# Kernel tuning notes

Measured on AMD Instinct MI355X. Metric: run time of the kernel, lower is better.

Reference implementation:

```python
import jax, jax.numpy as jnp
import numpy as np

T, A = 4096, 4          # tokens, atoms per token
N = T * A               # flat atoms
QB, KB = 32, 128        # query block / key window (AF3 atom transformer)
S = N // QB             # number of query subsets
H, DK = 4, 32           # heads, key dim per head
NB = 3                  # transformer blocks
CA, CP, CT = 128, 16, 384

# clipped sliding key window centered on each 32-atom query block
KIDX = jnp.clip(jnp.arange(S)[:, None] * QB - (KB - QB) // 2 + jnp.arange(KB)[None, :], 0, N - 1)

PARAM_SHAPES = [('w_ref_pos', (3, CA)), ('w_ref_mask', (1, CA)), ('w_ref_element', (CA, CA)), ('w_ref_charge', (1, CA)), ('w_ref_atom_name', (256, CA)), ('w_s2p_row', (CA, CP)), ('w_s2p_col', (CA, CP)), ('w_pair_offsets', (3, CP)), ('w_pair_dist', (1, CP)), ('w_pair_mask', (1, CP)), ('w_pair_mlp1', (CP, CP)), ('w_pair_mlp2', (CP, CP)), ('w_pair_mlp3', (CP, CP)), ('w_pair_ln', (CP,)), ('w_pair_logits', (CP, NB * H)), ('aq_lnw', (NB, CA)), ('aq_gw', (NB, CA, CA)), ('aq_gb', (NB, CA)), ('aq_sw', (NB, CA, CA)), ('ak_lnw', (NB, CA)), ('ak_gw', (NB, CA, CA)), ('ak_gb', (NB, CA)), ('ak_sw', (NB, CA, CA)), ('wq', (NB, CA, CA)), ('bq', (NB, CA)), ('wk', (NB, CA, CA)), ('wv', (NB, CA, CA)), ('wg', (NB, CA, CA)), ('azi_w', (NB, CA, CA)), ('azi_cw', (NB, CA, CA)), ('azi_cb', (NB, CA)), ('t_lnw', (NB, CA)), ('t_gw', (NB, CA, CA)), ('t_gb', (NB, CA)), ('t_sw', (NB, CA, CA)), ('glu1', (NB, CA, 2 * CA)), ('glu2', (NB, CA, 2 * CA)), ('t_azi_w', (NB, 2 * CA, CA)), ('t_azi_cw', (NB, CA, CA)), ('t_azi_cb', (NB, CA)), ('w_project', (CA, CT))]


def _ln(x, w=None, eps=1e-5):
    mu = jnp.mean(x, -1, keepdims=True)
    var = jnp.var(x, -1, keepdims=True)
    xn = (x - mu) * jax.lax.rsqrt(var + eps)
    return xn * w if w is not None else xn


def _ada_ln(x, cond, lnw, gw, gb, sw):
    c = _ln(cond, lnw)
    return jax.nn.sigmoid(c @ gw + gb) * _ln(x) + c @ sw


def setup_inputs() -> dict:
    ks = iter(jax.random.split(jax.random.key(0), 64))
    d = {}
    d['positions'] = jax.random.normal(next(ks), (T, A, 3), jnp.float32) * 3.0
    d['mask'] = jnp.ones((T, A), jnp.float32)
    d['element'] = jax.random.randint(next(ks), (T, A), 0, 128, jnp.int32)
    d['charge'] = jax.random.normal(next(ks), (T, A), jnp.float32)
    d['atom_name_chars'] = jax.random.randint(next(ks), (T, A, 4), 0, 64, jnp.int32)
    d['ref_space_uid'] = jax.random.randint(next(ks), (T, A), 0, T, jnp.int32)
    for nm, shp in PARAM_SHAPES:
        if nm.endswith('lnw') or nm == 'w_pair_ln':
            d[nm] = jnp.ones(shp, jnp.float32)
        else:
            d[nm] = jax.random.normal(next(ks), shp, jnp.float32) * 0.02
    return d


def _forward(positions, mask, charge, w_ref_pos, w_ref_mask, w_ref_element, w_ref_charge, w_ref_atom_name, w_s2p_row, w_s2p_col, w_pair_offsets, w_pair_dist, w_pair_mask, w_pair_mlp1, w_pair_mlp2, w_pair_mlp3, w_pair_ln, w_pair_logits, aq_lnw, aq_gw, aq_gb, aq_sw, ak_lnw, ak_gw, ak_gb, ak_sw, wq, bq, wk, wv, wg, azi_w, azi_cw, azi_cb, t_lnw, t_gw, t_gb, t_sw, glu1, glu2, t_azi_w, t_azi_cw, t_azi_cb, w_project, element, atom_name_chars, ref_space_uid):
    dt = positions.dtype
    pos = positions.reshape(N, 3)
    m = mask.reshape(N, 1)
    # per_atom_cond
    el1h = jax.nn.one_hot(element.reshape(N), 128, dtype=dt)
    nm1h = jax.nn.one_hot(atom_name_chars.reshape(N, 4), 64, dtype=dt).reshape(N, 256)
    ch = jnp.arcsinh(charge.reshape(N, 1))
    act = pos @ w_ref_pos + m @ w_ref_mask + el1h @ w_ref_element + ch @ w_ref_charge + nm1h @ w_ref_atom_name
    act = act * m
    qsc = act.reshape(S, QB, CA)  # queries_single_cond
    # pair conditioning
    uid = ref_space_uid.reshape(N)
    q_uid, k_uid = uid.reshape(S, QB), uid[KIDX]
    q_pos, k_pos = pos.reshape(S, QB, 3), pos[KIDX]
    valid = (q_uid[:, :, None] == k_uid[:, None, :]).astype(dt)[..., None]  # [S,QB,KB,1]
    off = q_pos[:, :, None, :] - k_pos[:, None, :, :]  # [S,QB,KB,3]
    pair = (off @ w_pair_offsets) * valid
    sq = jnp.sum(off * off, -1, keepdims=True)
    pair = pair + ((1.0 / (1.0 + sq)) @ w_pair_dist) * valid
    ksc = act[KIDX]  # keys_single_cond [S,KB,CA]
    pair = pair + (jax.nn.relu(qsc) @ w_s2p_row)[:, :, None, :] + (jax.nn.relu(ksc) @ w_s2p_col)[:, None, :, :]
    pair = pair + valid @ w_pair_mask
    t = jax.nn.relu(pair) @ w_pair_mlp1
    t = jax.nn.relu(t) @ w_pair_mlp2
    t = jax.nn.relu(t) @ w_pair_mlp3
    pair = pair + t
    # pair logits for all blocks: [NB, S, H, QB, KB]
    pl = (_ln(pair, w_pair_ln) @ w_pair_logits).reshape(S, QB, KB, NB, H)
    pl = jnp.transpose(pl, (3, 0, 4, 1, 2))
    qact = qsc
    scale = DK ** -0.5
    for i in range(NB):
        kact = qact.reshape(N, CA)[KIDX]
        xq = _ada_ln(qact, qsc, aq_lnw[i], aq_gw[i], aq_gb[i], aq_sw[i])
        xk = _ada_ln(kact, ksc, ak_lnw[i], ak_gw[i], ak_gb[i], ak_sw[i])
        q = (xq @ wq[i] + bq[i]).reshape(S, QB, H, DK)
        k = (xk @ wk[i]).reshape(S, KB, H, DK)
        logits = jnp.einsum('sqhd,skhd->shqk', q * scale, k) + pl[i]
        aw = jax.nn.softmax(logits, axis=-1)
        v = (xk @ wv[i]).reshape(S, KB, H, DK)
        o = jnp.einsum('shqk,skhd->sqhd', aw, v).reshape(S, QB, CA)
        o = o * jax.nn.sigmoid(xq @ wg[i])
        o = (o @ azi_w[i]) * jax.nn.sigmoid(qsc @ azi_cw[i] + azi_cb[i])  # AdaptiveZeroInit
        qact = qact + o
        xt = _ada_ln(qact, qsc, t_lnw[i], t_gw[i], t_gb[i], t_sw[i])
        xt = jax.nn.silu(xt @ glu1[i]) * (xt @ glu2[i])  # SwiGLU
        xt = (xt @ t_azi_w[i]) * jax.nn.sigmoid(qsc @ t_azi_cw[i] + t_azi_cb[i])
        qact = qact + xt
    tok = jax.nn.relu(qact.reshape(T, A, CA) @ w_project)
    mm = mask[..., None]
    token_act = jnp.sum(tok * mm, -2) / jnp.maximum(jnp.sum(mm, -2), 1e-10)
    return token_act, qact, qsc, pair


def reference(positions, mask, element, charge, atom_name_chars, ref_space_uid, w_ref_pos, w_ref_mask, w_ref_element, w_ref_charge, w_ref_atom_name, w_s2p_row, w_s2p_col, w_pair_offsets, w_pair_dist, w_pair_mask, w_pair_mlp1, w_pair_mlp2, w_pair_mlp3, w_pair_ln, w_pair_logits, aq_lnw, aq_gw, aq_gb, aq_sw, ak_lnw, ak_gw, ak_gb, ak_sw, wq, bq, wk, wv, wg, azi_w, azi_cw, azi_cb, t_lnw, t_gw, t_gb, t_sw, glu1, glu2, t_azi_w, t_azi_cw, t_azi_cb, w_project):
    return _forward(positions, mask, charge, w_ref_pos, w_ref_mask, w_ref_element, w_ref_charge, w_ref_atom_name, w_s2p_row, w_s2p_col, w_pair_offsets, w_pair_dist, w_pair_mask, w_pair_mlp1, w_pair_mlp2, w_pair_mlp3, w_pair_ln, w_pair_logits, aq_lnw, aq_gw, aq_gb, aq_sw, ak_lnw, ak_gw, ak_gb, ak_sw, wq, bq, wk, wv, wg, azi_w, azi_cw, azi_cb, t_lnw, t_gw, t_gb, t_sw, glu1, glu2, t_azi_w, t_azi_cw, t_azi_cb, w_project, element, atom_name_chars, ref_space_uid)
```

## Files before the change

kernel.cpp:

```cpp
#include <hip/hip_runtime.h>
#include <math.h>

#define TT 4096
#define AA 4
#define NN 16384
#define QBQ 32
#define KBK 128
#define SS 512
#define HH 4
#define DKD 32
#define CAC 128
#define CPC 16
#define CTC 384

typedef __attribute__((ext_vector_type(8))) short bf16x8;
typedef __attribute__((ext_vector_type(4))) short s16x4;
typedef __attribute__((ext_vector_type(4))) float f32x4;

__device__ __forceinline__ float sig_(float x) { return 1.0f / (1.0f + __expf(-x)); }
__device__ __forceinline__ short f2bf(float f) {
    unsigned u = __float_as_uint(f);
    unsigned r = (u + 0x7FFFu + ((u >> 16) & 1u)) >> 16;
    return (short)r;
}
__device__ __forceinline__ float b2f(short s) {
    return __uint_as_float(((unsigned)(unsigned short)s) << 16);
}

struct PEnt { const float* src; const float* rs; short* dst; int K; int NC; };
struct PTab { PEnt e[49]; };

__global__ __launch_bounds__(256) void k_prep(PTab tab)
{
    const PEnt e = tab.e[blockIdx.y];
    const int ntx = e.NC >> 5, nty = e.K >> 5, nt = ntx * nty;
    __shared__ float sm[32][33];
    const int lx = threadIdx.x & 31, ly = threadIdx.x >> 5;
    for (int t = blockIdx.x; t < nt; t += gridDim.x) {
        const int ty = t / ntx, tx = t - ty * ntx;
        #pragma unroll
        for (int j = 0; j < 4; ++j) {
            const int k = ty * 32 + ly + j * 8;
            const int n = tx * 32 + lx;
            float v = e.src[(size_t)k * e.NC + n];
            if (e.rs) v *= e.rs[k];
            sm[ly + j * 8][lx] = v;
        }
        __syncthreads();
        #pragma unroll
        for (int j = 0; j < 4; ++j) {
            const int n = tx * 32 + ly + j * 8;
            const int k = ty * 32 + lx;
            e.dst[(size_t)n * e.K + k] = f2bf(sm[lx][ly + j * 8]);
        }
        __syncthreads();
    }
}

__global__ __launch_bounds__(128) void k_atom_cond(
    const float* __restrict__ pos, const float* __restrict__ msk,
    const int* __restrict__ elem, const float* __restrict__ chg,
    const int* __restrict__ chars,
    const float* __restrict__ w_pos, const float* __restrict__ w_msk,
    const float* __restrict__ w_elem, const float* __restrict__ w_chg,
    const float* __restrict__ w_name,
    const float* __restrict__ w_row, const float* __restrict__ w_col,
    float* __restrict__ qsc, float* __restrict__ qact,
    short* __restrict__ qsc_bf, short* __restrict__ qn_bf,
    float* __restrict__ stats,
    float* __restrict__ rq, float* __restrict__ rk)
{
    const int n = blockIdx.x, c = threadIdx.x;
    const float p0 = pos[n*3+0], p1 = pos[n*3+1], p2 = pos[n*3+2];
    const float m = msk[n];
    const int   el = elem[n];
    const float ach = asinhf(chg[n]);
    const int c0 = chars[n*4+0], c1 = chars[n*4+1], c2 = chars[n*4+2], c3 = chars[n*4+3];

    float a = p0*w_pos[c] + p1*w_pos[CAC+c] + p2*w_pos[2*CAC+c]
            + m*w_msk[c] + w_elem[el*CAC+c] + ach*w_chg[c]
            + w_name[(c0      )*CAC+c] + w_name[( 64+c1)*CAC+c]
            + w_name[(128+c2)*CAC+c] + w_name[(192+c3)*CAC+c];
    a *= m;

    const size_t base = (size_t)n*CAC + c;
    qsc[base] = a; qact[base] = a; qsc_bf[base] = f2bf(a);

    __shared__ float red[128];
    __shared__ float sh[128];
    red[c] = a; __syncthreads();
    for (int off = 64; off > 0; off >>= 1) { if (c < off) red[c] += red[c+off]; __syncthreads(); }
    const float mu = red[0] * (1.0f/128.0f);
    __syncthreads();
    const float d = a - mu;
    red[c] = d*d; __syncthreads();
    for (int off = 64; off > 0; off >>= 1) { if (c < off) red[c] += red[c+off]; __syncthreads(); }
    const float var = red[0] * (1.0f/128.0f);
    const float rs = rsqrtf(var + 1e-5f);
    qn_bf[base] = f2bf(d * rs);
    if (c == 0) { stats[2*n] = mu; stats[2*n+1] = rs; }
    __syncthreads();
    sh[c] = fmaxf(a, 0.0f);
    __syncthreads();
    if (c < 32) {
        const float* w = (c < 16) ? w_row : w_col;
        const int cc = c & 15;
        float acc = 0.0f;
        #pragma unroll 8
        for (int r = 0; r < 128; ++r) acc += sh[r] * w[r*CPC + cc];
        if (c < 16) rq[(size_t)n*CPC + cc] = acc;
        else        rk[(size_t)n*CPC + cc] = acc;
    }
}

__global__ __launch_bounds__(256) void k_pair(
    const float* __restrict__ pos, const int* __restrict__ uid,
    const float* __restrict__ rq, const float* __restrict__ rk,
    const float* __restrict__ w_ofs, const float* __restrict__ w_dist,
    const float* __restrict__ w_pm,
    const float* __restrict__ mlp1, const float* __restrict__ mlp2,
    const float* __restrict__ mlp3,
    const float* __restrict__ wln, const float* __restrict__ wpl,
    float* __restrict__ pair, short* __restrict__ plb)
{
    __shared__ float sm1[256], sm2[256], sm3[256], sofs[48], sdist[16], smask[16];
    __shared__ float swln[16], swpl[192];
    const int tid = threadIdx.x;
    sm1[tid] = mlp1[tid]; sm2[tid] = mlp2[tid]; sm3[tid] = mlp3[tid];
    if (tid < 48) sofs[tid] = w_ofs[tid];
    if (tid < 16) { sdist[tid] = w_dist[tid]; smask[tid] = w_pm[tid]; swln[tid] = wln[tid]; }
    if (tid < 192) swpl[tid] = wpl[tid];
    __syncthreads();

    const int gid = blockIdx.x*256 + tid;
    const int s = gid >> 12;
    const int rem = gid & 4095;
    const int q = rem >> 7, kk = rem & 127;
    const int n = s*QBQ + q;
    int kidx = s*QBQ - 48 + kk; kidx = max(0, min(NN-1, kidx));

    const float v = (uid[n] == uid[kidx]) ? 1.0f : 0.0f;
    const float o0 = pos[n*3+0]-pos[kidx*3+0];
    const float o1 = pos[n*3+1]-pos[kidx*3+1];
    const float o2 = pos[n*3+2]-pos[kidx*3+2];
    const float sq = o0*o0 + o1*o1 + o2*o2;
    const float inv = 1.0f/(1.0f + sq);

    const float* rqp = rq + (size_t)n*CPC;
    const float* rkp = rk + (size_t)kidx*CPC;

    float p[16], t1[16], t2[16];
    #pragma unroll
    for (int j = 0; j < 16; ++j)
        p[j] = v*(o0*sofs[j] + o1*sofs[16+j] + o2*sofs[32+j] + inv*sdist[j] + smask[j])
             + rqp[j] + rkp[j];
    #pragma unroll
    for (int j = 0; j < 16; ++j) {
        float acc = 0.0f;
        #pragma unroll
        for (int r = 0; r < 16; ++r) acc += fmaxf(p[r], 0.0f) * sm1[r*16+j];
        t1[j] = acc;
    }
    #pragma unroll
    for (int j = 0; j < 16; ++j) {
        float acc = 0.0f;
        #pragma unroll
        for (int r = 0; r < 16; ++r) acc += fmaxf(t1[r], 0.0f) * sm2[r*16+j];
        t2[j] = acc;
    }
    #pragma unroll
    for (int j = 0; j < 16; ++j) {
        float acc = 0.0f;
        #pragma unroll
        for (int r = 0; r < 16; ++r) acc += fmaxf(t2[r], 0.0f) * sm3[r*16+j];
        t1[j] = p[j] + acc;
    }
    float* op = pair + (size_t)gid*CPC;
    #pragma unroll
    for (int j = 0; j < 4; ++j)
        *(float4*)(op + j*4) = make_float4(t1[j*4], t1[j*4+1], t1[j*4+2], t1[j*4+3]);

    float sm = 0.0f;
    #pragma unroll
    for (int j = 0; j < 16; ++j) sm += t1[j];
    const float mu = sm * (1.0f/16.0f);
    float vq = 0.0f;
    #pragma unroll
    for (int j = 0; j < 16; ++j) { const float dd = t1[j]-mu; vq += dd*dd; }
    const float rs = rsqrtf(vq*(1.0f/16.0f) + 1e-5f);
    float xn[16];
    #pragma unroll
    for (int j = 0; j < 16; ++j) xn[j] = (t1[j]-mu)*rs*swln[j];
    #pragma unroll
    for (int i = 0; i < 3; ++i) {
        #pragma unroll
        for (int h = 0; h < 4; ++h) {
            float acc = 0.0f;
            #pragma unroll
            for (int j = 0; j < 16; ++j) acc += xn[j] * swpl[j*12 + i*4 + h];
            plb[((((size_t)i*SS + s)*HH + h)*QBQ + q)*KBK + kk] = f2bf(acc);
        }
    }
}

struct FJob {
    const void* A; const void* A2;
    const float* stats; const short* G; const short* S;
    const short* Bt; const float* bias;
    float* outF; short* outB;
    const short* gate; float* resid; float* ostats;
    int K; int ostride; int amode; int emode;
};
struct FJobs { FJob j[8]; };

__global__ __launch_bounds__(256) void k_mmf(FJobs jobs)
{
    __shared__ short As[128*64];
    __shared__ short Bs[128*64];
    const FJob J = jobs.j[blockIdx.y];
    const int tid = threadIdx.x;
    const int wave = tid >> 6, lane = tid & 63;
    const int l15 = lane & 15, l4 = lane >> 4;
    const int row0 = blockIdx.x * 128;
    const int K = J.K;

    f32x4 acc[2][8];
    #pragma unroll
    for (int m = 0; m < 2; ++m)
        #pragma unroll
        for (int n = 0; n < 8; ++n) acc[m][n] = (f32x4){0.f,0.f,0.f,0.f};

    for (int k0 = 0; k0 < K; k0 += 64) {
        #pragma unroll
        for (int j = 0; j < 4; ++j) {
            const int u = tid + j*256;
            const int r = u >> 3, ug = u & 7;
            const int row = row0 + r;
            const size_t ao = (size_t)row*K + k0 + ug*8;
            bf16x8 av;
            if (J.amode == 0) {
                av = *(const bf16x8*)((const short*)J.A + ao);
            } else if (J.amode == 1) {
                const float* Af = (const float*)J.A;
                const float4 a0 = *(const float4*)(Af + ao);
                const float4 a1 = *(const float4*)(Af + ao + 4);
                const float mu = J.stats[2*row], rs = J.stats[2*row+1];
                const s16x4 g0 = *(const s16x4*)(J.G + ao), g1 = *(const s16x4*)(J.G + ao + 4);
                const s16x4 s0 = *(const s16x4*)(J.S + ao), s1 = *(const s16x4*)(J.S + ao + 4);
                const float x[8] = {a0.x,a0.y,a0.z,a0.w,a1.x,a1.y,a1.z,a1.w};
                #pragma unroll
                for (int t = 0; t < 4; ++t) {
                    av[t]   = f2bf(b2f(g0[t])*((x[t]  -mu)*rs) + b2f(s0[t]));
                    av[t+4] = f2bf(b2f(g1[t])*((x[t+4]-mu)*rs) + b2f(s1[t]));
                }
            } else if (J.amode == 2) {
                const float* Ao = (const float*)J.A;
                const float* Ag = (const float*)J.A2;
                const float4 oa = *(const float4*)(Ao + ao);
                const float4 ob = *(const float4*)(Ao + ao + 4);
                const float4 ga = *(const float4*)(Ag + ao);
                const float4 gb = *(const float4*)(Ag + ao + 4);
                av[0]=f2bf(oa.x*ga.x); av[1]=f2bf(oa.y*ga.y); av[2]=f2bf(oa.z*ga.z); av[3]=f2bf(oa.w*ga.w);
                av[4]=f2bf(ob.x*gb.x); av[5]=f2bf(ob.y*gb.y); av[6]=f2bf(ob.z*gb.z); av[7]=f2bf(ob.w*gb.w);
            } else {
                const float* Af = (const float*)J.A;
                const float4 a0 = *(const float4*)(Af + ao);
                const float4 a1 = *(const float4*)(Af + ao + 4);
                av[0]=f2bf(a0.x); av[1]=f2bf(a0.y); av[2]=f2bf(a0.z); av[3]=f2bf(a0.w);
                av[4]=f2bf(a1.x); av[5]=f2bf(a1.y); av[6]=f2bf(a1.z); av[7]=f2bf(a1.w);
            }
            *(bf16x8*)&As[r*64 + ((ug ^ (r & 7)) * 8)] = av;
            const bf16x8 bv = *(const bf16x8*)(J.Bt + (size_t)r*K + k0 + ug*8);
            *(bf16x8*)&Bs[r*64 + ((ug ^ (r & 7)) * 8)] = bv;
        }
        __syncthreads();
        #pragma unroll
        for (int ks = 0; ks < 2; ++ks) {
            bf16x8 af[2], bfr[8];
            #pragma unroll
            for (int m = 0; m < 2; ++m) {
                const int r = wave*32 + m*16 + l15;
                af[m] = *(const bf16x8*)&As[r*64 + (((ks*4 + l4) ^ (r & 7)) * 8)];
            }
            #pragma unroll
            for (int n = 0; n < 8; ++n) {
                const int c = n*16 + l15;
                bfr[n] = *(const bf16x8*)&Bs[c*64 + (((ks*4 + l4) ^ (c & 7)) * 8)];
            }
            #pragma unroll
            for (int m = 0; m < 2; ++m)
                #pragma unroll
                for (int n = 0; n < 8; ++n)
                    acc[m][n] = __builtin_amdgcn_mfma_f32_16x16x32_bf16(af[m], bfr[n], acc[m][n], 0, 0, 0);
        }
        __syncthreads();
    }

    if (J.emode == 3) {
        #pragma unroll
        for (int m = 0; m < 2; ++m) {
            #pragma unroll
            for (int reg = 0; reg < 4; ++reg) {
                const int row = row0 + wave*32 + m*16 + l4*4 + reg;
                float s = 0.0f, q = 0.0f;
                #pragma unroll
                for (int n = 0; n < 8; ++n) {
                    const int col = n*16 + l15;
                    const size_t off = (size_t)row*CAC + col;
                    const float v = J.resid[off] + acc[m][n][reg] * b2f(J.gate[off]);
                    J.resid[off] = v;
                    s += v; q += v*v;
                }
                #pragma unroll
                for (int msk = 1; msk < 16; msk <<= 1) {
                    s += __shfl_xor(s, msk, 64);
                    q += __shfl_xor(q, msk, 64);
                }
                if (l15 == 0) {
                    const float mu = s * (1.0f/128.0f);
                    const float var = q * (1.0f/128.0f) - mu*mu;
                    J.ostats[2*row]   = mu;
                    J.ostats[2*row+1] = rsqrtf(var + 1e-5f);
                }
            }
        }
    } else {
        float bval[8];
        #pragma unroll
        for (int n = 0; n < 8; ++n) bval[n] = 0.0f;
        if (J.bias) {
            #pragma unroll
            for (int n = 0; n < 8; ++n) bval[n] = J.bias[n*16 + l15];
        }
        const int epi = J.emode;
        #pragma unroll
        for (int m = 0; m < 2; ++m) {
            #pragma unroll
            for (int n = 0; n < 8; ++n) {
                const int col = n*16 + l15;
                #pragma unroll
                for (int reg = 0; reg < 4; ++reg) {
                    const int row = row0 + wave*32 + m*16 + l4*4 + reg;
                    float v = acc[m][n][reg] + bval[n];
                    if (epi == 1) v = sig_(v);
                    if (epi == 2) v = fmaxf(v, 0.0f);
                    if (J.outB) J.outB[(size_t)row*J.ostride + col] = f2bf(v);
                    else        J.outF[(size_t)row*J.ostride + col] = v;
                }
            }
        }
    }
}

__global__ __launch_bounds__(256) void k_mm_glu(
    const float* __restrict__ qact, const float* __restrict__ stats,
    const short* __restrict__ Gt, const short* __restrict__ St,
    const short* __restrict__ B1t, const short* __restrict__ B2t,
    short* __restrict__ out)
{
    __shared__ short As[128*64];
    __shared__ short B1s[64*64];
    __shared__ short B2s[64*64];
    const int tid = threadIdx.x;
    const int wave = tid >> 6, lane = tid & 63;
    const int l15 = lane & 15, l4 = lane >> 4;
    const int row0 = blockIdx.x * 128;
    const int col0 = blockIdx.y * 64;

    f32x4 acc1[2][4], acc2[2][4];
    #pragma unroll
    for (int m = 0; m < 2; ++m)
        #pragma unroll
        for (int n = 0; n < 4; ++n) {
            acc1[m][n] = (f32x4){0.f,0.f,0.f,0.f};
            acc2[m][n] = (f32x4){0.f,0.f,0.f,0.f};
        }

    for (int k0 = 0; k0 < 128; k0 += 64) {
        #pragma unroll
        for (int j = 0; j < 4; ++j) {
            const int u = tid + j*256;
            const int r = u >> 3, ug = u & 7;
            const int row = row0 + r;
            const size_t ao = (size_t)row*CAC + k0 + ug*8;
            const float4 a0 = *(const float4*)(qact + ao);
            const float4 a1 = *(const float4*)(qact + ao + 4);
            const float mu = stats[2*row], rs = stats[2*row+1];
            const s16x4 g0 = *(const s16x4*)(Gt + ao), g1 = *(const s16x4*)(Gt + ao + 4);
            const s16x4 s0 = *(const s16x4*)(St + ao), s1 = *(const s16x4*)(St + ao + 4);
            const float x[8] = {a0.x,a0.y,a0.z,a0.w,a1.x,a1.y,a1.z,a1.w};
            bf16x8 av;
            #pragma unroll
            for (int t = 0; t < 4; ++t) {
                av[t]   = f2bf(b2f(g0[t])*((x[t]  -mu)*rs) + b2f(s0[t]));
                av[t+4] = f2bf(b2f(g1[t])*((x[t+4]-mu)*rs) + b2f(s1[t]));
            }
            *(bf16x8*)&As[r*64 + ((ug ^ (r & 7)) * 8)] = av;
        }
        #pragma unroll
        for (int j = 0; j < 2; ++j) {
            const int u = tid + j*256;
            const int r = u >> 3, ug = u & 7;
            const bf16x8 b1 = *(const bf16x8*)(B1t + (size_t)(col0 + r)*128 + k0 + ug*8);
            *(bf16x8*)&B1s[r*64 + ((ug ^ (r & 7)) * 8)] = b1;
            const bf16x8 b2 = *(const bf16x8*)(B2t + (size_t)(col0 + r)*128 + k0 + ug*8);
            *(bf16x8*)&B2s[r*64 + ((ug ^ (r & 7)) * 8)] = b2;
        }
        __syncthreads();
        #pragma unroll
        for (int ks = 0; ks < 2; ++ks) {
            bf16x8 af[2], bq1[4], bq2[4];
            #pragma unroll
            for (int m = 0; m < 2; ++m) {
                const int r = wave*32 + m*16 + l15;
                af[m] = *(const bf16x8*)&As[r*64 + (((ks*4 + l4) ^ (r & 7)) * 8)];
            }
            #pragma unroll
            for (int n = 0; n < 4; ++n) {
                const int c = n*16 + l15;
                bq1[n] = *(const bf16x8*)&B1s[c*64 + (((ks*4 + l4) ^ (c & 7)) * 8)];
                bq2[n] = *(const bf16x8*)&B2s[c*64 + (((ks*4 + l4) ^ (c & 7)) * 8)];
            }
            #pragma unroll
            for (int m = 0; m < 2; ++m)
                #pragma unroll
                for (int n = 0; n < 4; ++n) {
                    acc1[m][n] = __builtin_amdgcn_mfma_f32_16x16x32_bf16(af[m], bq1[n], acc1[m][n], 0, 0, 0);
                    acc2[m][n] = __builtin_amdgcn_mfma_f32_16x16x32_bf16(af[m], bq2[n], acc2[m][n], 0, 0, 0);
                }
        }
        __syncthreads();
    }

    #pragma unroll
    for (int m = 0; m < 2; ++m)
        #pragma unroll
        for (int n = 0; n < 4; ++n) {
            const int col = col0 + n*16 + l15;
            #pragma unroll
            for (int reg = 0; reg < 4; ++reg) {
                const int row = row0 + wave*32 + m*16 + l4*4 + reg;
                const float a1 = acc1[m][n][reg];
                const float h = a1 * sig_(a1) * acc2[m][n][reg];
                out[(size_t)row*256 + col] = f2bf(h);
            }
        }
}

__global__ __launch_bounds__(512) void k_attn2(
    const float* __restrict__ qh, const float* __restrict__ kh,
    const float* __restrict__ vh, const short* __restrict__ pls,
    float* __restrict__ oh)
{
    __shared__ float sm_m[256], sm_l[256], sm_acc[256*17];
    const int s = blockIdx.x, tid = threadIdx.x;
    const int kh2 = tid >> 8;
    const int h = (tid >> 6) & 3;
    const int q = (tid >> 1) & 31;
    const int dh = tid & 1;
    const int n0 = s*QBQ;
    const int kbase = n0 - 48 + kh2*64;
    const float SCALE = 0.17677669529663687f;

    float qr[32];
    {
        const float* qp = qh + (size_t)(n0+q)*CAC + h*DKD;
        #pragma unroll
        for (int j = 0; j < 8; ++j) {
            const float4 v4 = *(const float4*)(qp + j*4);
            qr[j*4]=v4.x*SCALE; qr[j*4+1]=v4.y*SCALE; qr[j*4+2]=v4.z*SCALE; qr[j*4+3]=v4.w*SCALE;
        }
    }
    const short* plp = pls + (((size_t)s*HH + h)*QBQ + q)*KBK + kh2*64;

    float m = -1e30f, l = 0.0f;
    float acc[16];
    #pragma unroll
    for (int j = 0; j < 16; ++j) acc[j] = 0.0f;

    for (int kb4 = 0; kb4 < 16; ++kb4) {
        const s16x4 p4 = *(const s16x4*)(plp + kb4*4);
        float pv[4];
        #pragma unroll
        for (int j = 0; j < 4; ++j) pv[j] = b2f(p4[j]);
        #pragma unroll
        for (int j = 0; j < 4; ++j) {
            const int kb = kb4*4 + j;
            int kidx = kbase + kb; kidx = max(0, min(NN-1, kidx));
            const float* kp = kh + (size_t)kidx*CAC + h*DKD;
            float dot = 0.0f;
            #pragma unroll
            for (int jj = 0; jj < 8; ++jj) {
                const float4 kv = *(const float4*)(kp + jj*4);
                dot += qr[jj*4]*kv.x + qr[jj*4+1]*kv.y + qr[jj*4+2]*kv.z + qr[jj*4+3]*kv.w;
            }
            const float sv = dot + pv[j];
            if (sv > m) {
                const float corr = __expf(m - sv);
                l *= corr;
                #pragma unroll
                for (int d = 0; d < 16; ++d) acc[d] *= corr;
                m = sv;
            }
            const float w = __expf(sv - m);
            l += w;
            const float* vp = vh + (size_t)kidx*CAC + h*DKD + dh*16;
            #pragma unroll
            for (int jj = 0; jj < 4; ++jj) {
                const float4 vv = *(const float4*)(vp + jj*4);
                acc[jj*4]   = fmaf(w, vv.x, acc[jj*4]);
                acc[jj*4+1] = fmaf(w, vv.y, acc[jj*4+1]);
                acc[jj*4+2] = fmaf(w, vv.z, acc[jj*4+2]);
                acc[jj*4+3] = fmaf(w, vv.w, acc[jj*4+3]);
            }
        }
    }

    const int part = tid & 255;
    if (kh2 == 1) {
        sm_m[part] = m; sm_l[part] = l;
        #pragma unroll
        for (int j = 0; j < 16; ++j) sm_acc[part*17 + j] = acc[j];
    }
    __syncthreads();
    if (kh2 == 0) {
        const float m2 = sm_m[part], l2 = sm_l[part];
        const float mm = fmaxf(m, m2);
        const float c1 = __expf(m - mm), c2 = __expf(m2 - mm);
        const float inv = 1.0f / (l*c1 + l2*c2);
        float* op = oh + (size_t)(n0+q)*CAC + h*DKD + dh*16;
        #pragma unroll
        for (int jj = 0; jj < 4; ++jj) {
            float o0 = (acc[jj*4  ]*c1 + sm_acc[part*17+jj*4  ]*c2) * inv;
            float o1 = (acc[jj*4+1]*c1 + sm_acc[part*17+jj*4+1]*c2) * inv;
            float o2 = (acc[jj*4+2]*c1 + sm_acc[part*17+jj*4+2]*c2) * inv;
            float o3 = (acc[jj*4+3]*c1 + sm_acc[part*17+jj*4+3]*c2) * inv;
            *(float4*)op = make_float4(o0,o1,o2,o3);
            op += 4;
        }
    }
}

__global__ __launch_bounds__(256) void k_token_reduce(
    const float* __restrict__ tok, const float* __restrict__ msk, float* __restrict__ out)
{
    const int gid = blockIdx.x*256 + threadIdx.x;
    const int t = gid / CTC, c = gid - t*CTC;
    float num = 0.0f, den = 0.0f;
    #pragma unroll
    for (int a = 0; a < AA; ++a) {
        const float mv = msk[t*AA + a];
        num += tok[(size_t)(t*AA+a)*CTC + c] * mv;
        den += mv;
    }
    out[gid] = num / fmaxf(den, 1e-10f);
}

static inline FJob fj0() { FJob j{}; return j; }

extern "C" void kernel_launch(void* const* d_in, const int* in_sizes, int n_in,
                              void* d_out, int out_size, void* d_ws, size_t ws_size,
                              hipStream_t stream)
{
    const float* positions = (const float*)d_in[0];
    const float* maskp     = (const float*)d_in[1];
    const int*   element   = (const int*  )d_in[2];
    const float* charge    = (const float*)d_in[3];
    const int*   chars     = (const int*  )d_in[4];
    const int*   uid       = (const int*  )d_in[5];
    const float* w_ref_pos      = (const float*)d_in[6];
    const float* w_ref_mask     = (const float*)d_in[7];
    const float* w_ref_element  = (const float*)d_in[8];
    const float* w_ref_charge   = (const float*)d_in[9];
    const float* w_ref_atom_name= (const float*)d_in[10];
    const float* w_s2p_row      = (const float*)d_in[11];
    const float* w_s2p_col      = (const float*)d_in[12];
    const float* w_pair_offsets = (const float*)d_in[13];
    const float* w_pair_dist    = (const float*)d_in[14];
    const float* w_pair_mask    = (const float*)d_in[15];
    const float* w_pair_mlp1    = (const float*)d_in[16];
    const float* w_pair_mlp2    = (const float*)d_in[17];
    const float* w_pair_mlp3    = (const float*)d_in[18];
    const float* w_pair_ln      = (const float*)d_in[19];
    const float* w_pair_logits  = (const float*)d_in[20];
    const float* aq_lnw = (const float*)d_in[21];
    const float* aq_gw  = (const float*)d_in[22];
    const float* aq_gb  = (const float*)d_in[23];
    const float* aq_sw  = (const float*)d_in[24];
    const float* ak_lnw = (const float*)d_in[25];
    const float* ak_gw  = (const float*)d_in[26];
    const float* ak_gb  = (const float*)d_in[27];
    const float* ak_sw  = (const float*)d_in[28];
    const float* wq     = (const float*)d_in[29];
    const float* bq     = (const float*)d_in[30];
    const float* wk     = (const float*)d_in[31];
    const float* wv     = (const float*)d_in[32];
    const float* wg     = (const float*)d_in[33];
    const float* azi_w  = (const float*)d_in[34];
    const float* azi_cw = (const float*)d_in[35];
    const float* azi_cb = (const float*)d_in[36];
    const float* t_lnw  = (const float*)d_in[37];
    const float* t_gw   = (const float*)d_in[38];
    const float* t_gb   = (const float*)d_in[39];
    const float* t_sw   = (const float*)d_in[40];
    const float* glu1   = (const float*)d_in[41];
    const float* glu2   = (const float*)d_in[42];
    const float* t_azi_w  = (const float*)d_in[43];
    const float* t_azi_cw = (const float*)d_in[44];
    const float* t_azi_cb = (const float*)d_in[45];
    const float* w_project= (const float*)d_in[46];

    float* token_o = (float*)d_out;
    float* qact = token_o + 1572864;
    float* qsc  = token_o + 3670016;
    float* pair = token_o + 5767168;

    char* W = (char*)d_ws;
    short* pl_bf   = (short*)(W);
    short* wbf     = (short*)(W + 50331648);
    short* qn_bf   = (short*)(W + 52428800);
    short* qsc_bf  = (short*)(W + 56623104);
    float* stats   = (float*)(W + 60817408);
    short* Gq_bf   = (short*)(W + 60948480);
    short* Sq_bf   = (short*)(W + 65142784);
    short* Gk_bf   = (short*)(W + 69337088);
    short* Sk_bf   = (short*)(W + 73531392);
    short* Gt_bf   = (short*)(W + 77725696);
    short* St_bf   = (short*)(W + 81920000);
    short* Ag_bf   = (short*)(W + 86114304);
    short* Tg_bf   = (short*)(W + 90308608);
    float* w_q     = (float*)(W + 94502912);
    float* w_k     = (float*)(W + 102891520);
    float* w_v     = (float*)(W + 111280128);
    float* w_g     = (float*)(W + 119668736);
    float* w_o     = (float*)(W + 128057344);
    short* hs_bf   = (short*)(W + 136445952);
    float* rq      = (float*)(W + 144834560);
    float* rk      = (float*)(W + 145883136);
    float* tok = w_q;

    (void)in_sizes; (void)n_in; (void)out_size; (void)ws_size;

    const size_t LSTR = 311296;
    const size_t oGQ=0, oSQ=16384, oGK=32768, oSK=49152, oGT=65536, oST=81920,
                 oWQ=98304, oWK=114688, oWV=131072, oWG=147456, oAZ=163840,
                 oACW=180224, oTCW=196608, oG1=212992, oG2=245760, oTAW=278528;
    const size_t oPROJ = 3*LSTR;

    {
        PTab tab{};
        int e = 0;
        for (int i = 0; i < 3; ++i) {
            short* L = wbf + (size_t)i*LSTR;
            const size_t oM = (size_t)i*CAC*CAC, oV = (size_t)i*CAC, oGL = (size_t)i*CAC*2*CAC;
            tab.e[e++] = {aq_gw+oM,  aq_lnw+oV, L+oGQ,  128, 128};
            tab.e[e++] = {aq_sw+oM,  aq_lnw+oV, L+oSQ,  128, 128};
            tab.e[e++] = {ak_gw+oM,  ak_lnw+oV, L+oGK,  128, 128};
            tab.e[e++] = {ak_sw+oM,  ak_lnw+oV, L+oSK,  128, 128};
            tab.e[e++] = {t_gw+oM,   t_lnw+oV,  L+oGT,  128, 128};
            tab.e[e++] = {t_sw+oM,   t_lnw+oV,  L+oST,  128, 128};
            tab.e[e++] = {wq+oM,     nullptr,   L+oWQ,  128, 128};
            tab.e[e++] = {wk+oM,     nullptr,   L+oWK,  128, 128};
            tab.e[e++] = {wv+oM,     nullptr,   L+oWV,  128, 128};
            tab.e[e++] = {wg+oM,     nullptr,   L+oWG,  128, 128};
            tab.e[e++] = {azi_w+oM,  nullptr,   L+oAZ,  128, 128};
            tab.e[e++] = {azi_cw+oM, nullptr,   L+oACW, 128, 128};
            tab.e[e++] = {t_azi_cw+oM,nullptr,  L+oTCW, 128, 128};
            tab.e[e++] = {glu1+oGL,  nullptr,   L+oG1,  128, 256};
            tab.e[e++] = {glu2+oGL,  nullptr,   L+oG2,  128, 256};
            tab.e[e++] = {t_azi_w+oGL,nullptr,  L+oTAW, 256, 128};
        }
        tab.e[e++] = {w_project, nullptr, wbf+oPROJ, 128, 384};
        k_prep<<<dim3(48, 49), 256, 0, stream>>>(tab);
    }

    k_atom_cond<<<NN, 128, 0, stream>>>(positions, maskp, element, charge, chars,
        w_ref_pos, w_ref_mask, w_ref_element, w_ref_charge, w_ref_atom_name,
        w_s2p_row, w_s2p_col, qsc, qact, qsc_bf, qn_bf, stats, rq, rk);

    k_pair<<<(SS*QBQ*KBK)/256, 256, 0, stream>>>(positions, uid, rq, rk,
        w_pair_offsets, w_pair_dist, w_pair_mask, w_pair_mlp1, w_pair_mlp2, w_pair_mlp3,
        w_pair_ln, w_pair_logits, pair, pl_bf);

    for (int i = 0; i < 3; ++i) {
        short* L = wbf + (size_t)i*LSTR;
        const size_t oV = (size_t)i*CAC;

        {
            FJobs js{};
            struct { const short* A; const short* Bt; const float* bias; short* out; int em; } cfg[8] = {
                {qn_bf,  L+oGQ,  aq_gb+oV,    Gq_bf, 1}, {qn_bf,  L+oSQ,  nullptr, Sq_bf, 0},
                {qn_bf,  L+oGK,  ak_gb+oV,    Gk_bf, 1}, {qn_bf,  L+oSK,  nullptr, Sk_bf, 0},
                {qn_bf,  L+oGT,  t_gb+oV,     Gt_bf, 1}, {qn_bf,  L+oST,  nullptr, St_bf, 0},
                {qsc_bf, L+oACW, azi_cb+oV,   Ag_bf, 1}, {qsc_bf, L+oTCW, t_azi_cb+oV, Tg_bf, 1}};
            for (int jn = 0; jn < 8; ++jn) {
                FJob j = fj0();
                j.A = cfg[jn].A; j.Bt = cfg[jn].Bt; j.bias = cfg[jn].bias;
                j.outB = cfg[jn].out; j.K = 128; j.ostride = 128;
                j.amode = 0; j.emode = cfg[jn].em;
                js.j[jn] = j;
            }
            k_mmf<<<dim3(128, 8), 256, 0, stream>>>(js);
        }
        {
            FJobs js{};
            struct { const short* G; const short* S; const short* Bt; const float* bias; float* out; int em; } cfg[4] = {
                {Gq_bf, Sq_bf, L+oWQ, bq+oV,   w_q, 0}, {Gk_bf, Sk_bf, L+oWK, nullptr, w_k, 0},
                {Gk_bf, Sk_bf, L+oWV, nullptr, w_v, 0}, {Gq_bf, Sq_bf, L+oWG, nullptr, w_g, 1}};
            for (int jn = 0; jn < 4; ++jn) {
                FJob j = fj0();
                j.A = qact; j.stats = stats; j.G = cfg[jn].G; j.S = cfg[jn].S;
                j.Bt = cfg[jn].Bt; j.bias = cfg[jn].bias; j.outF = cfg[jn].out;
                j.K = 128; j.ostride = 128; j.amode = 1; j.emode = cfg[jn].em;
                js.j[jn] = j;
            }
            k_mmf<<<dim3(128, 4), 256, 0, stream>>>(js);
        }
        k_attn2<<<SS, 512, 0, stream>>>(w_q, w_k, w_v, pl_bf + (size_t)i*8388608, w_o);
        {
            FJobs js{};
            FJob j = fj0();
            j.A = w_o; j.A2 = w_g; j.Bt = L+oAZ;
            j.gate = Ag_bf; j.resid = qact; j.ostats = stats;
            j.K = 128; j.ostride = 128; j.amode = 2; j.emode = 3;
            js.j[0] = j;
            k_mmf<<<dim3(128, 1), 256, 0, stream>>>(js);
        }
        k_mm_glu<<<dim3(128, 4), 256, 0, stream>>>(qact, stats, Gt_bf, St_bf, L+oG1, L+oG2, hs_bf);
        {
            FJobs js{};
            FJob j = fj0();
            j.A = hs_bf; j.Bt = L+oTAW;
            j.gate = Tg_bf; j.resid = qact; j.ostats = stats;
            j.K = 256; j.ostride = 128; j.amode = 0; j.emode = 3;
            js.j[0] = j;
            k_mmf<<<dim3(128, 1), 256, 0, stream>>>(js);
        }
    }

    {
        FJobs js{};
        for (int c = 0; c < 3; ++c) {
            FJob j = fj0();
            j.A = qact; j.Bt = wbf + oPROJ + (size_t)c*16384;
            j.outF = tok + c*128;
            j.K = 128; j.ostride = 384; j.amode = 3; j.emode = 2;
            js.j[c] = j;
        }
        k_mmf<<<dim3(128, 3), 256, 0, stream>>>(js);
    }
    k_token_reduce<<<(TT*CTC)/256, 256, 0, stream>>>(tok, maskp, token_o);
}
```

Measured before the change: 933.9 us.

## Fuse QKVG GEMMs with shared A tile, retile GEMMs, stage pair stores through LDS

Adds a dedicated k_mm_qkvg kernel that builds the adaLN-normalized A tile once per q/k side and multiplies it by two weight matrices, so the normalization is no longer redone for each of the four projections. k_mmf becomes templated on its row-tile size, and the single-job GEMMs run with 64-row tiles to launch more blocks. k_mm_glu widens its column tile to 128 so each A tile is reused across more output columns. In k_pair, rq/rk are read with vector loads and pair outputs go through shared memory so the global writes are coalesced. The trade-off is higher register and LDS use, and more blocks, which may lower occupancy.

After: 996.7 us. +6.7%, slower.

```diff
diff --git a/kernel.cpp b/kernel.cpp
--- a/kernel.cpp
+++ b/kernel.cpp
@@ -125,6 +125,7 @@
 {
     __shared__ float sm1[256], sm2[256], sm3[256], sofs[48], sdist[16], smask[16];
     __shared__ float swln[16], swpl[192];
+    __shared__ float st[256*17];
     const int tid = threadIdx.x;
     sm1[tid] = mlp1[tid]; sm2[tid] = mlp2[tid]; sm3[tid] = mlp3[tid];
     if (tid < 48) sofs[tid] = w_ofs[tid];
@@ -148,12 +149,20 @@
 
     const float* rqp = rq + (size_t)n*CPC;
     const float* rkp = rk + (size_t)kidx*CPC;
+    float rqv[16], rkv[16];
+    #pragma unroll
+    for (int j = 0; j < 4; ++j) {
+        const float4 a = *(const float4*)(rqp + j*4);
+        const float4 b = *(const float4*)(rkp + j*4);
+        rqv[j*4]=a.x; rqv[j*4+1]=a.y; rqv[j*4+2]=a.z; rqv[j*4+3]=a.w;
+        rkv[j*4]=b.x; rkv[j*4+1]=b.y; rkv[j*4+2]=b.z; rkv[j*4+3]=b.w;
+    }
 
     float p[16], t1[16], t2[16];
     #pragma unroll
     for (int j = 0; j < 16; ++j)
         p[j] = v*(o0*sofs[j] + o1*sofs[16+j] + o2*sofs[32+j] + inv*sdist[j] + smask[j])
-             + rqp[j] + rkp[j];
+             + rqv[j] + rkv[j];
     #pragma unroll
     for (int j = 0; j < 16; ++j) {
         float acc = 0.0f;
@@ -175,10 +184,8 @@
         for (int r = 0; r < 16; ++r) acc += fmaxf(t2[r], 0.0f) * sm3[r*16+j];
         t1[j] = p[j] + acc;
     }
-    float* op = pair + (size_t)gid*CPC;
-    #pragma unroll
-    for (int j = 0; j < 4; ++j)
-        *(float4*)(op + j*4) = make_float4(t1[j*4], t1[j*4+1], t1[j*4+2], t1[j*4+3]);
+    #pragma unroll
+    for (int j = 0; j < 16; ++j) st[tid*17 + j] = t1[j];
 
     float sm = 0.0f;
     #pragma unroll
@@ -200,6 +207,13 @@
             for (int j = 0; j < 16; ++j) acc += xn[j] * swpl[j*12 + i*4 + h];
             plb[((((size_t)i*SS + s)*HH + h)*QBQ + q)*KBK + kk] = f2bf(acc);
         }
+    }
+    __syncthreads();
+    float4* bb = (float4*)(pair + (size_t)blockIdx.x*256*CPC);
+    #pragma unroll
+    for (int l = tid; l < 1024; l += 256) {
+        const int e = l >> 2, jj = (l & 3) * 4;
+        bb[l] = make_float4(st[e*17+jj], st[e*17+jj+1], st[e*17+jj+2], st[e*17+jj+3]);
     }
 }
 
@@ -213,26 +227,27 @@
 };
 struct FJobs { FJob j[8]; };
 
+template<int MF>
 __global__ __launch_bounds__(256) void k_mmf(FJobs jobs)
 {
-    __shared__ short As[128*64];
+    __shared__ short As[MF*64*64];
     __shared__ short Bs[128*64];
     const FJob J = jobs.j[blockIdx.y];
     const int tid = threadIdx.x;
     const int wave = tid >> 6, lane = tid & 63;
     const int l15 = lane & 15, l4 = lane >> 4;
-    const int row0 = blockIdx.x * 128;
+    const int row0 = blockIdx.x * (MF*64);
     const int K = J.K;
 
-    f32x4 acc[2][8];
-    #pragma unroll
-    for (int m = 0; m < 2; ++m)
+    f32x4 acc[MF][8];
+    #pragma unroll
+    for (int m = 0; m < MF; ++m)
         #pragma unroll
         for (int n = 0; n < 8; ++n) acc[m][n] = (f32x4){0.f,0.f,0.f,0.f};
 
     for (int k0 = 0; k0 < K; k0 += 64) {
         #pragma unroll
-        for (int j = 0; j < 4; ++j) {
+        for (int j = 0; j < MF*2; ++j) {
             const int u = tid + j*256;
             const int r = u >> 3, ug = u & 7;
             const int row = row0 + r;
@@ -240,19 +255,6 @@
             bf16x8 av;
             if (J.amode == 0) {
                 av = *(const bf16x8*)((const short*)J.A + ao);
-            } else if (J.amode == 1) {
-                const float* Af = (const float*)J.A;
-                const float4 a0 = *(const float4*)(Af + ao);
-                const float4 a1 = *(const float4*)(Af + ao + 4);
-                const float mu = J.stats[2*row], rs = J.stats[2*row+1];
-                const s16x4 g0 = *(const s16x4*)(J.G + ao), g1 = *(const s16x4*)(J.G + ao + 4);
-                const s16x4 s0 = *(const s16x4*)(J.S + ao), s1 = *(const s16x4*)(J.S + ao + 4);
-                const float x[8] = {a0.x,a0.y,a0.z,a0.w,a1.x,a1.y,a1.z,a1.w};
-                #pragma unroll
-                for (int t = 0; t < 4; ++t) {
-                    av[t]   = f2bf(b2f(g0[t])*((x[t]  -mu)*rs) + b2f(s0[t]));
-                    av[t+4] = f2bf(b2f(g1[t])*((x[t+4]-mu)*rs) + b2f(s1[t]));
-                }
             } else if (J.amode == 2) {
                 const float* Ao = (const float*)J.A;
                 const float* Ag = (const float*)J.A2;
@@ -270,16 +272,21 @@
                 av[4]=f2bf(a1.x); av[5]=f2bf(a1.y); av[6]=f2bf(a1.z); av[7]=f2bf(a1.w);
             }
             *(bf16x8*)&As[r*64 + ((ug ^ (r & 7)) * 8)] = av;
-            const bf16x8 bv = *(const bf16x8*)(J.Bt + (size_t)r*K + k0 + ug*8);
-            *(bf16x8*)&Bs[r*64 + ((ug ^ (r & 7)) * 8)] = bv;
+        }
+        #pragma unroll
+        for (int j = 0; j < 4; ++j) {
+            const int u = tid + j*256;
+            const int r = u >> 3, ug = u & 7;
+            *(bf16x8*)&Bs[r*64 + ((ug ^ (r & 7)) * 8)] =
+                *(const bf16x8*)(J.Bt + (size_t)r*K + k0 + ug*8);
         }
         __syncthreads();
         #pragma unroll
         for (int ks = 0; ks < 2; ++ks) {
-            bf16x8 af[2], bfr[8];
-            #pragma unroll
-            for (int m = 0; m < 2; ++m) {
-                const int r = wave*32 + m*16 + l15;
+            bf16x8 af[MF], bfr[8];
+            #pragma unroll
+            for (int m = 0; m < MF; ++m) {
+                const int r = wave*(16*MF) + m*16 + l15;
                 af[m] = *(const bf16x8*)&As[r*64 + (((ks*4 + l4) ^ (r & 7)) * 8)];
             }
             #pragma unroll
@@ -288,7 +295,7 @@
                 bfr[n] = *(const bf16x8*)&Bs[c*64 + (((ks*4 + l4) ^ (c & 7)) * 8)];
             }
             #pragma unroll
-            for (int m = 0; m < 2; ++m)
+            for (int m = 0; m < MF; ++m)
                 #pragma unroll
                 for (int n = 0; n < 8; ++n)
                     acc[m][n] = __builtin_amdgcn_mfma_f32_16x16x32_bf16(af[m], bfr[n], acc[m][n], 0, 0, 0);
@@ -298,10 +305,10 @@
 
     if (J.emode == 3) {
         #pragma unroll
-        for (int m = 0; m < 2; ++m) {
+        for (int m = 0; m < MF; ++m) {
             #pragma unroll
             for (int reg = 0; reg < 4; ++reg) {
-                const int row = row0 + wave*32 + m*16 + l4*4 + reg;
+                const int row = row0 + wave*(16*MF) + m*16 + l4*4 + reg;
                 float s = 0.0f, q = 0.0f;
                 #pragma unroll
                 for (int n = 0; n < 8; ++n) {
@@ -334,13 +341,13 @@
         }
         const int epi = J.emode;
         #pragma unroll
-        for (int m = 0; m < 2; ++m) {
+        for (int m = 0; m < MF; ++m) {
             #pragma unroll
             for (int n = 0; n < 8; ++n) {
                 const int col = n*16 + l15;
                 #pragma unroll
                 for (int reg = 0; reg < 4; ++reg) {
-                    const int row = row0 + wave*32 + m*16 + l4*4 + reg;
+                    const int row = row0 + wave*(16*MF) + m*16 + l4*4 + reg;
                     float v = acc[m][n][reg] + bval[n];
                     if (epi == 1) v = sig_(v);
                     if (epi == 2) v = fmaxf(v, 0.0f);
@@ -350,6 +357,108 @@
             }
         }
     }
+}
+
+__global__ __launch_bounds__(256) void k_mm_qkvg(
+    const float* __restrict__ qact, const float* __restrict__ stats,
+    const short* __restrict__ Gq, const short* __restrict__ Sq,
+    const short* __restrict__ Gk, const short* __restrict__ Sk,
+    const short* __restrict__ Btq, const short* __restrict__ Btg,
+    const short* __restrict__ Btk, const short* __restrict__ Btv,
+    const float* __restrict__ bq,
+    float* __restrict__ w_q, float* __restrict__ w_k,
+    float* __restrict__ w_v, float* __restrict__ w_g)
+{
+    __shared__ short As[128*64];
+    __shared__ short B1s[128*64];
+    __shared__ short B2s[128*64];
+    const int tid = threadIdx.x;
+    const int wave = tid >> 6, lane = tid & 63;
+    const int l15 = lane & 15, l4 = lane >> 4;
+    const int row0 = blockIdx.x * 128;
+    const bool qside = (blockIdx.y == 0);
+    const short* G  = qside ? Gq : Gk;
+    const short* S  = qside ? Sq : Sk;
+    const short* B1 = qside ? Btq : Btk;
+    const short* B2 = qside ? Btg : Btv;
+    float* O1 = qside ? w_q : w_k;
+    float* O2 = qside ? w_g : w_v;
+
+    f32x4 acc1[2][8], acc2[2][8];
+    #pragma unroll
+    for (int m = 0; m < 2; ++m)
+        #pragma unroll
+        for (int n = 0; n < 8; ++n) {
+            acc1[m][n] = (f32x4){0.f,0.f,0.f,0.f};
+            acc2[m][n] = (f32x4){0.f,0.f,0.f,0.f};
+        }
+
+    for (int k0 = 0; k0 < 128; k0 += 64) {
+        #pragma unroll
+        for (int j = 0; j < 4; ++j) {
+            const int u = tid + j*256;
+            const int r = u >> 3, ug = u & 7;
+            const int row = row0 + r;
+            const size_t ao = (size_t)row*CAC + k0 + ug*8;
+            const float4 a0 = *(const float4*)(qact + ao);
+            const float4 a1 = *(const float4*)(qact + ao + 4);
+            const float mu = stats[2*row], rs = stats[2*row+1];
+            const s16x4 g0 = *(const s16x4*)(G + ao), g1 = *(const s16x4*)(G + ao + 4);
+            const s16x4 s0 = *(const s16x4*)(S + ao), s1 = *(const s16x4*)(S + ao + 4);
+            const float x[8] = {a0.x,a0.y,a0.z,a0.w,a1.x,a1.y,a1.z,a1.w};
+            bf16x8 av;
+            #pragma unroll
+            for (int t = 0; t < 4; ++t) {
+                av[t]   = f2bf(b2f(g0[t])*((x[t]  -mu)*rs) + b2f(s0[t]));
+                av[t+4] = f2bf(b2f(g1[t])*((x[t+4]-mu)*rs) + b2f(s1[t]));
+            }
+            const int sw = (ug ^ (r & 7)) * 8;
+            *(bf16x8*)&As[r*64 + sw] = av;
+            const size_t bo = (size_t)r*CAC + k0 + ug*8;
+            *(bf16x8*)&B1s[r*64 + sw] = *(const bf16x8*)(B1 + bo);
+            *(bf16x8*)&B2s[r*64 + sw] = *(const bf16x8*)(B2 + bo);
+        }
+        __syncthreads();
+        #pragma unroll
+        for (int ks = 0; ks < 2; ++ks) {
+            bf16x8 af[2], b1f[8], b2f_[8];
+            #pragma unroll
+            for (int m = 0; m < 2; ++m) {
+                const int r = wave*32 + m*16 + l15;
+                af[m] = *(const bf16x8*)&As[r*64 + (((ks*4 + l4) ^ (r & 7)) * 8)];
+            }
+            #pragma unroll
+            for (int n = 0; n < 8; ++n) {
+                const int c = n*16 + l15;
+                const int sw = ((ks*4 + l4) ^ (c & 7)) * 8;
+                b1f[n] = *(const bf16x8*)&B1s[c*64 + sw];
+                b2f_[n] = *(const bf16x8*)&B2s[c*64 + sw];
+            }
+            #pragma unroll
+            for (int m = 0; m < 2; ++m)
+                #pragma unroll
+                for (int n = 0; n < 8; ++n) {
+                    acc1[m][n] = __builtin_amdgcn_mfma_f32_16x16x32_bf16(af[m], b1f[n], acc1[m][n], 0, 0, 0);
+                    acc2[m][n] = __builtin_amdgcn_mfma_f32_16x16x32_bf16(af[m], b2f_[n], acc2[m][n], 0, 0, 0);
+                }
+        }
+        __syncthreads();
+    }
+
+    #pragma unroll
+    for (int m = 0; m < 2; ++m)
+        #pragma unroll
+        for (int n = 0; n < 8; ++n) {
+            const int col = n*16 + l15;
+            const float bv = qside ? bq[col] : 0.0f;
+            #pragma unroll
+            for (int reg = 0; reg < 4; ++reg) {
+                const int row = row0 + wave*32 + m*16 + l4*4 + reg;
+                O1[(size_t)row*CAC + col] = acc1[m][n][reg] + bv;
+                const float v2 = acc2[m][n][reg];
+                O2[(size_t)row*CAC + col] = qside ? sig_(v2) : v2;
+            }
+        }
 }
 
 __global__ __launch_bounds__(256) void k_mm_glu(
@@ -359,19 +468,19 @@
     short* __restrict__ out)
 {
     __shared__ short As[128*64];
-    __shared__ short B1s[64*64];
-    __shared__ short B2s[64*64];
+    __shared__ short B1s[128*64];
+    __shared__ short B2s[128*64];
     const int tid = threadIdx.x;
     const int wave = tid >> 6, lane = tid & 63;
     const int l15 = lane & 15, l4 = lane >> 4;
     const int row0 = blockIdx.x * 128;
-    const int col0 = blockIdx.y * 64;
-
-    f32x4 acc1[2][4], acc2[2][4];
+    const int col0 = blockIdx.y * 128;
+
+    f32x4 acc1[2][8], acc2[2][8];
     #pragma unroll
     for (int m = 0; m < 2; ++m)
         #pragma unroll
-        for (int n = 0; n < 4; ++n) {
+        for (int n = 0; n < 8; ++n) {
             acc1[m][n] = (f32x4){0.f,0.f,0.f,0.f};
             acc2[m][n] = (f32x4){0.f,0.f,0.f,0.f};
         }
@@ -395,38 +504,34 @@
                 av[t]   = f2bf(b2f(g0[t])*((x[t]  -mu)*rs) + b2f(s0[t]));
                 av[t+4] = f2bf(b2f(g1[t])*((x[t+4]-mu)*rs) + b2f(s1[t]));
             }
-            *(bf16x8*)&As[r*64 + ((ug ^ (r & 7)) * 8)] = av;
-        }
-        #pragma unroll
-        for (int j = 0; j < 2; ++j) {
-            const int u = tid + j*256;
-            const int r = u >> 3, ug = u & 7;
-            const bf16x8 b1 = *(const bf16x8*)(B1t + (size_t)(col0 + r)*128 + k0 + ug*8);
-            *(bf16x8*)&B1s[r*64 + ((ug ^ (r & 7)) * 8)] = b1;
-            const bf16x8 b2 = *(const bf16x8*)(B2t + (size_t)(col0 + r)*128 + k0 + ug*8);
-            *(bf16x8*)&B2s[r*64 + ((ug ^ (r & 7)) * 8)] = b2;
+            const int sw = (ug ^ (r & 7)) * 8;
+            *(bf16x8*)&As[r*64 + sw] = av;
+            const size_t bo = (size_t)(col0 + r)*CAC + k0 + ug*8;
+            *(bf16x8*)&B1s[r*64 + sw] = *(const bf16x8*)(B1t + bo);
+            *(bf16x8*)&B2s[r*64 + sw] = *(const bf16x8*)(B2t + bo);
         }
         __syncthreads();
         #pragma unroll
         for (int ks = 0; ks < 2; ++ks) {
-            bf16x8 af[2], bq1[4], bq2[4];
+            bf16x8 af[2], b1f[8], b2f_[8];
             #pragma unroll
             for (int m = 0; m < 2; ++m) {
                 const int r = wave*32 + m*16 + l15;
                 af[m] = *(const bf16x8*)&As[r*64 + (((ks*4 + l4) ^ (r & 7)) * 8)];
             }
             #pragma unroll
-            for (int n = 0; n < 4; ++n) {
+            for (int n = 0; n < 8; ++n) {
                 const int c = n*16 + l15;
-                bq1[n] = *(const bf16x8*)&B1s[c*64 + (((ks*4 + l4) ^ (c & 7)) * 8)];
-                bq2[n] = *(const bf16x8*)&B2s[c*64 + (((ks*4 + l4) ^ (c & 7)) * 8)];
+                const int sw = ((ks*4 + l4) ^ (c & 7)) * 8;
+                b1f[n] = *(const bf16x8*)&B1s[c*64 + sw];
+                b2f_[n] = *(const bf16x8*)&B2s[c*64 + sw];
             }
             #pragma unroll
             for (int m = 0; m < 2; ++m)
                 #pragma unroll
-                for (int n = 0; n < 4; ++n) {
-                    acc1[m][n] = __builtin_amdgcn_mfma_f32_16x16x32_bf16(af[m], bq1[n], acc1[m][n], 0, 0, 0);
-                    acc2[m][n] = __builtin_amdgcn_mfma_f32_16x16x32_bf16(af[m], bq2[n], acc2[m][n], 0, 0, 0);
+                for (int n = 0; n < 8; ++n) {
+                    acc1[m][n] = __builtin_amdgcn_mfma_f32_16x16x32_bf16(af[m], b1f[n], acc1[m][n], 0, 0, 0);
+                    acc2[m][n] = __builtin_amdgcn_mfma_f32_16x16x32_bf16(af[m], b2f_[n], acc2[m][n], 0, 0, 0);
                 }
         }
         __syncthreads();
@@ -435,14 +540,13 @@
     #pragma unroll
     for (int m = 0; m < 2; ++m)
         #pragma unroll
-        for (int n = 0; n < 4; ++n) {
+        for (int n = 0; n < 8; ++n) {
             const int col = col0 + n*16 + l15;
             #pragma unroll
             for (int reg = 0; reg < 4; ++reg) {
                 const int row = row0 + wave*32 + m*16 + l4*4 + reg;
                 const float a1 = acc1[m][n][reg];
-                const float h = a1 * sig_(a1) * acc2[m][n][reg];
-                out[(size_t)row*256 + col] = f2bf(h);
+                out[(size_t)row*256 + col] = f2bf(a1 * sig_(a1) * acc2[m][n][reg]);
             }
         }
 }
@@ -700,22 +804,11 @@
                 j.amode = 0; j.emode = cfg[jn].em;
                 js.j[jn] = j;
             }
-            k_mmf<<<dim3(128, 8), 256, 0, stream>>>(js);
-        }
-        {
-            FJobs js{};
-            struct { const short* G; const short* S; const short* Bt; const float* bias; float* out; int em; } cfg[4] = {
-                {Gq_bf, Sq_bf, L+oWQ, bq+oV,   w_q, 0}, {Gk_bf, Sk_bf, L+oWK, nullptr, w_k, 0},
-                {Gk_bf, Sk_bf, L+oWV, nullptr, w_v, 0}, {Gq_bf, Sq_bf, L+oWG, nullptr, w_g, 1}};
-            for (int jn = 0; jn < 4; ++jn) {
-                FJob j = fj0();
-                j.A = qact; j.stats = stats; j.G = cfg[jn].G; j.S = cfg[jn].S;
-                j.Bt = cfg[jn].Bt; j.bias = cfg[jn].bias; j.outF = cfg[jn].out;
-                j.K = 128; j.ostride = 128; j.amode = 1; j.emode = cfg[jn].em;
-                js.j[jn] = j;
-            }
-            k_mmf<<<dim3(128, 4), 256, 0, stream>>>(js);
-        }
+            k_mmf<2><<<dim3(128, 8), 256, 0, stream>>>(js);
+        }
+        k_mm_qkvg<<<dim3(128, 2), 256, 0, stream>>>(qact, stats,
+            Gq_bf, Sq_bf, Gk_bf, Sk_bf, L+oWQ, L+oWG, L+oWK, L+oWV,
+            bq+oV, w_q, w_k, w_v, w_g);
         k_attn2<<<SS, 512, 0, stream>>>(w_q, w_k, w_v, pl_bf + (size_t)i*8388608, w_o);
         {
             FJobs js{};
@@ -724,9 +817,9 @@
             j.gate = Ag_bf; j.resid = qact; j.ostats = stats;
             j.K = 128; j.ostride = 128; j.amode = 2; j.emode = 3;
             js.j[0] = j;
-            k_mmf<<<dim3(128, 1), 256, 0, stream>>>(js);
-        }
-        k_mm_glu<<<dim3(128, 4), 256, 0, stream>>>(qact, stats, Gt_bf, St_bf, L+oG1, L+oG2, hs_bf);
+            k_mmf<1><<<dim3(256, 1), 256, 0, stream>>>(js);
+        }
+        k_mm_glu<<<dim3(128, 2), 256, 0, stream>>>(qact, stats, Gt_bf, St_bf, L+oG1, L+oG2, hs_bf);
         {
             FJobs js{};
             FJob j = fj0();
@@ -734,7 +827,7 @@
             j.gate = Tg_bf; j.resid = qact; j.ostats = stats;
             j.K = 256; j.ostride = 128; j.amode = 0; j.emode = 3;
             js.j[0] = j;
-            k_mmf<<<dim3(128, 1), 256, 0, stream>>>(js);
+            k_mmf<1><<<dim3(256, 1), 256, 0, stream>>>(js);
         }
     }
 
@@ -747,7 +840,7 @@
             j.K = 128; j.ostride = 384; j.amode = 3; j.emode = 2;
             js.j[c] = j;
         }
-        k_mmf<<<dim3(128, 3), 256, 0, stream>>>(js);
+        k_mmf<1><<<dim3(256, 3), 256, 0, stream>>>(js);
     }
     k_token_reduce<<<(TT*CTC)/256, 256, 0, stream>>>(tok, maskp, token_o);
 }
```
